# Optimization experiments

Measured on AMD Instinct MI355X. Metric: run time of the kernel, lower is better.

Reference implementation:

```python
import jax, jax.numpy as jnp
import numpy as np
from jax import lax

B, S, D_MODEL, H, D_CONV, CHUNK = 8, 4096, 1024, 16, 4, 64
D_INNER = D_MODEL


def setup_inputs() -> dict:
    key = jax.random.key(0)
    ks = jax.random.split(key, 6)
    x = jax.random.normal(ks[0], (B, S, D_MODEL), jnp.float32)
    in_proj_w = jax.random.normal(ks[1], (D_INNER + H, D_MODEL), jnp.float32) * 0.02
    conv_w = jax.random.normal(ks[2], (D_INNER, 1, D_CONV), jnp.float32) * 0.3
    conv_b = jnp.zeros((D_INNER,), jnp.float32)
    w_base = jax.random.uniform(ks[3], (H,), jnp.float32, minval=-0.5, maxval=0.5)
    out_proj_w = jax.random.normal(ks[4], (D_MODEL, D_INNER), jnp.float32) * 0.02
    return {"x": x, "in_proj_w": in_proj_w, "conv_w": conv_w, "conv_b": conv_b,
            "w_base": w_base, "out_proj_w": out_proj_w}


def _segsum(a):
    # a: (..., T) -> (..., T, T) with out[i, j] = sum_{k=j+1..i} a[k] for i>=j else -inf
    T = a.shape[-1]
    lower_strict = jnp.tril(jnp.ones((T, T), bool), -1)   # row i > col j
    lower = jnp.tril(jnp.ones((T, T), bool), 0)
    xr = jnp.where(lower_strict, a[..., :, None], 0.0)    # (..., T, T)
    s = jnp.cumsum(xr, axis=-2)
    return jnp.where(lower, s, -jnp.inf)


def _ssd(x, A, l):
    # x: (b, s, h, n); A: (b, s, h); l = chunk size
    b, s, h, n = x.shape
    c = s // l
    x = x.reshape(b, c, l, h, n)
    A = A.reshape(b, c, l, h).transpose(0, 3, 1, 2)        # (b, h, c, l)
    A_cumsum = jnp.cumsum(A, axis=-1)

    # intra-chunk (diagonal) part
    L_log = _segsum(A)                                      # (b, h, c, l, l)
    L = jnp.exp(L_log - jnp.max(L_log, axis=-1, keepdims=True))
    norm_diag = L.sum(-1).transpose(0, 2, 3, 1)             # (b, c, l, h)
    Y_diag = jnp.einsum('bhcls,bcshn->bclhn', L, x)

    # chunk states
    decay_states = A_cumsum[..., -1:] - A_cumsum            # (b, h, c, l)
    decay_states = jnp.exp(decay_states - jnp.max(decay_states, axis=-1, keepdims=True))
    norm_decay = decay_states.sum(-1).transpose(0, 2, 1)    # (b, c, h)
    states = jnp.einsum('bhcl,bclhn->bchn', decay_states, x)

    norm_decay = jnp.pad(norm_decay, ((0, 0), (1, 0), (0, 0)))
    states = jnp.pad(states, ((0, 0), (1, 0), (0, 0), (0, 0)))

    # inter-chunk recurrence
    decay_chunk = _segsum(jnp.pad(A_cumsum[..., -1], ((0, 0), (0, 0), (1, 0))))  # (b,h,c+1,c+1)
    decay_chunk = jnp.exp(decay_chunk - jnp.max(decay_chunk, axis=-1, keepdims=True))
    norm_decay = jnp.einsum('bhzc,bch->bzh', decay_chunk, norm_decay)[:, :-1]    # (b, c, h)
    states = jnp.einsum('bhzc,bchn->bzhn', decay_chunk, states)[:, :-1]          # (b, c, h, n)

    # off-diagonal output
    state_decay_out = jnp.exp(A_cumsum - jnp.max(A_cumsum, axis=-1, keepdims=True))
    norm_off = jnp.einsum('bch,bhcl->bclh', norm_decay, state_decay_out)
    Y_off = jnp.einsum('bchn,bhcl->bclhn', states, state_decay_out)

    Y = (Y_diag + Y_off).reshape(b, s, h, n)
    norm = (norm_diag + norm_off).reshape(b, s, h)
    return Y / norm[..., None]


def reference(x, in_proj_w, conv_w, conv_b, w_base, out_proj_w):
    b, s, d_model = x.shape
    d_inner = in_proj_w.shape[0] - H
    xw = jnp.einsum('bsd,ed->bse', x, in_proj_w)            # (b, s, d_inner + H)
    xi, w = xw[..., :d_inner], xw[..., d_inner:]            # (b,s,d_inner), (b,s,H)
    # causal depthwise conv (padding k-1 on the left == pad both + slice [:s])
    xc = lax.conv_general_dilated(
        xi.transpose(0, 2, 1), conv_w, window_strides=(1,),
        padding=[(D_CONV - 1, 0)], feature_group_count=d_inner,
        dimension_numbers=('NCH', 'OIH', 'NCH'))
    xc = (xc + conv_b[None, :, None]).transpose(0, 2, 1)    # (b, s, d_inner)
    xh = xc.reshape(b, s, H, d_inner // H)                  # (b, s, h, n)
    A = w * w_base                                          # (b, s, H)
    y = _ssd(xh, A, CHUNK)                                  # (b, s, h, n)
    y = y.reshape(b, s, d_inner)
    return jnp.einsum('bsd,ed->bse', y, out_proj_w)         # (b, s, d_model)
```

## Files before the change

kernel.cpp:

```cpp
#include <hip/hip_runtime.h>
#include <hip/hip_bf16.h>
#include <cstdint>

#define B_ 8
#define S_ 4096
#define DM 1024
#define H_ 16
#define DN 64
#define CH 64
#define NC 64
#define M_ (B_ * S_)

typedef unsigned short u16;
typedef u16 u16x8 __attribute__((ext_vector_type(8)));
typedef u16 u16x4 __attribute__((ext_vector_type(4)));
typedef float f32x4 __attribute__((ext_vector_type(4)));
typedef __bf16 bf16x8 __attribute__((ext_vector_type(8)));

__device__ __forceinline__ float bf2f(u16 u) { return __uint_as_float(((unsigned)u) << 16); }
__device__ __forceinline__ u16 f2bf(float f) { __bf16 h = (__bf16)f; return __builtin_bit_cast(u16, h); }

#define GLOAD16(gp, lp) \
  __builtin_amdgcn_global_load_lds((__attribute__((address_space(1))) const void*)(gp), \
                                   (__attribute__((address_space(3))) void*)(lp), 16, 0, 0)
#define BAR()   asm volatile("s_barrier" ::: "memory")
#define VMCNT6() asm volatile("s_waitcnt vmcnt(6)" ::: "memory")
#define VMCNT0() asm volatile("s_waitcnt vmcnt(0)" ::: "memory")

__device__ __forceinline__ void stage_unit(const u16* __restrict__ src, int row0, int kt,
                                           int ks, u16* ldsu, int t, int K) {
#pragma unroll
  for (int i = 0; i < 2; ++i) {
    int f = i * 512 + t;
    int row = f >> 2, j = f & 3;
    int g = j ^ ((row >> 1) & 3);
    GLOAD16(src + (size_t)(row0 + row) * K + kt * 64 + ks * 32 + g * 8, ldsu + f * 8);
  }
}

__device__ __forceinline__ void lda4(bf16x8* fr, const u16* unit, int rbase, int lr, int lk) {
#pragma unroll
  for (int q = 0; q < 4; ++q) {
    int row = rbase + q * 16 + lr;
    int cell = row * 4 + (lk ^ ((row >> 1) & 3));
    fr[q] = *reinterpret_cast<const bf16x8*>(&unit[cell * 8]);
  }
}

__device__ __forceinline__ void mfma16(f32x4 (&acc)[8][4], int mh, const bf16x8* aF, const bf16x8* bF) {
  __builtin_amdgcn_s_setprio(1);
#pragma unroll
  for (int q = 0; q < 4; ++q)
#pragma unroll
    for (int nf = 0; nf < 4; ++nf)
      acc[mh * 4 + q][nf] = __builtin_amdgcn_mfma_f32_16x16x32_bf16(aF[q], bF[nf], acc[mh * 4 + q][nf], 0, 0, 0);
  __builtin_amdgcn_s_setprio(0);
}

template<int MODE>
__global__ __launch_bounds__(512, 2) void bgemm8(
    const u16* __restrict__ A, const u16* __restrict__ Bw,
    void* __restrict__ Cout, int K)
{
  __shared__ u16 lds[8][8192];
  const int orig = blockIdx.x;
  const int swz  = (orig & 7) * 64 + (orig >> 3);
  const int m0 = (swz >> 2) * 256;
  const int n0 = (swz & 3) * 256;
  const int t  = threadIdx.x;
  const int wid = t >> 6, l = t & 63;
  const int wm = wid >> 2, wn = wid & 3;
  const int lr = l & 15, lk = l >> 4;
  const int arb = wm * 128;
  const int brb = wn * 64;

  f32x4 acc[8][4];
#pragma unroll
  for (int i = 0; i < 8; ++i)
#pragma unroll
    for (int j = 0; j < 4; ++j) acc[i][j] = (f32x4){0.f, 0.f, 0.f, 0.f};

  stage_unit(A,  m0, 0, 0, lds[0], t, K);
  stage_unit(A,  m0, 0, 1, lds[1], t, K);
  stage_unit(Bw, n0, 0, 0, lds[2], t, K);
  stage_unit(Bw, n0, 0, 1, lds[3], t, K);
  stage_unit(Bw, n0, 1, 0, lds[6], t, K);
  stage_unit(Bw, n0, 1, 1, lds[7], t, K);
  stage_unit(A,  m0, 1, 0, lds[4], t, K);
  VMCNT6();
  BAR();

  bf16x8 aF[4], bF0[4], bF1[4];
  for (int i = 0; i < 8; ++i) {
    const bool st = (i < 7);
    lda4(aF, lds[0], arb, lr, lk);
    lda4(bF0, lds[2], brb, lr, lk);
    stage_unit(A, m0, 2 * i + 1, 1, lds[5], t, K);
    BAR(); mfma16(acc, 0, aF, bF0); BAR();
    lda4(aF, lds[1], arb, lr, lk);
    lda4(bF1, lds[3], brb, lr, lk);
    if (st) stage_unit(Bw, n0, 2 * i + 2, 0, lds[2], t, K);
    BAR(); mfma16(acc, 0, aF, bF1); BAR();
    lda4(aF, lds[0], arb + 64, lr, lk);
    if (st) stage_unit(Bw, n0, 2 * i + 2, 1, lds[3], t, K);
    BAR(); mfma16(acc, 1, aF, bF0); BAR();
    lda4(aF, lds[1], arb + 64, lr, lk);
    if (st) { stage_unit(A, m0, 2 * i + 2, 0, lds[0], t, K); VMCNT6(); }
    else    { VMCNT0(); }
    BAR(); mfma16(acc, 1, aF, bF1); BAR();
    lda4(aF, lds[4], arb, lr, lk);
    lda4(bF0, lds[6], brb, lr, lk);
    if (st) stage_unit(A, m0, 2 * i + 2, 1, lds[1], t, K);
    BAR(); mfma16(acc, 0, aF, bF0); BAR();
    lda4(aF, lds[5], arb, lr, lk);
    lda4(bF1, lds[7], brb, lr, lk);
    if (st) stage_unit(Bw, n0, 2 * i + 3, 0, lds[6], t, K);
    BAR(); mfma16(acc, 0, aF, bF1); BAR();
    lda4(aF, lds[4], arb + 64, lr, lk);
    if (st) stage_unit(Bw, n0, 2 * i + 3, 1, lds[7], t, K);
    BAR(); mfma16(acc, 1, aF, bF0); BAR();
    lda4(aF, lds[5], arb + 64, lr, lk);
    if (st) { stage_unit(A, m0, 2 * i + 3, 0, lds[4], t, K); VMCNT6(); }
    BAR(); mfma16(acc, 1, aF, bF1); BAR();
  }

#pragma unroll
  for (int mf = 0; mf < 8; ++mf) {
#pragma unroll
    for (int nf = 0; nf < 4; ++nf) {
      int n  = n0 + wn * 64 + nf * 16 + lr;
      int mb = m0 + wm * 128 + mf * 16 + lk * 4;
#pragma unroll
      for (int r = 0; r < 4; ++r) {
        if (MODE == 0) ((float*)Cout)[(size_t)(mb + r) * 1024 + n] = acc[mf][nf][r];
        else           ((u16*)Cout)[(size_t)(mb + r) * 1024 + n] = f2bf(acc[mf][nf][r]);
      }
    }
  }
}

__global__ __launch_bounds__(256) void cvt32to16(const float* __restrict__ in, u16* __restrict__ out)
{
  size_t i = ((size_t)blockIdx.x * 256 + threadIdx.x) * 8;
  f32x4 a = *reinterpret_cast<const f32x4*>(&in[i]);
  f32x4 b = *reinterpret_cast<const f32x4*>(&in[i + 4]);
  u16x8 o;
#pragma unroll
  for (int j = 0; j < 4; ++j) { o[j] = f2bf(a[j]); o[4 + j] = f2bf(b[j]); }
  *reinterpret_cast<u16x8*>(&out[i]) = o;
}

__global__ __launch_bounds__(256) void cvtlo(const float* __restrict__ ipw, u16* __restrict__ wlo)
{
  size_t e = ((size_t)blockIdx.x * 256 + threadIdx.x) * 8;
  f32x4 a = *reinterpret_cast<const f32x4*>(&ipw[1048576 + e]);
  f32x4 b = *reinterpret_cast<const f32x4*>(&ipw[1048576 + e + 4]);
  u16x8 o;
#pragma unroll
  for (int j = 0; j < 4; ++j) {
    u16 h = f2bf(a[j]); o[j]     = f2bf(a[j] - bf2f(h));
    u16 g = f2bf(b[j]); o[4 + j] = f2bf(b[j] - bf2f(g));
  }
  *reinterpret_cast<u16x8*>(&wlo[e]) = o;
}

__global__ __launch_bounds__(256) void wsplit(
    const float* __restrict__ x, const u16* __restrict__ wbf, const u16* __restrict__ wlo,
    u16* __restrict__ xbf, float* __restrict__ wbufT)
{
  __shared__ u16 hi[64 * 64];
  __shared__ u16 lo[64 * 64];
  const int r0 = blockIdx.x * 64;
  const int t  = threadIdx.x;
  const int w  = t >> 6, l = t & 63;
  const int lr = l & 15, lk = l >> 4;
  const int c8   = t & 7;
  const int srow = t >> 3;

  f32x4 acc = (f32x4){0.f, 0.f, 0.f, 0.f};

  for (int kt = 0; kt < 16; ++kt) {
    __syncthreads();
#pragma unroll
    for (int p = 0; p < 2; ++p) {
      int row = srow + 32 * p;
      const float* gp = &x[(size_t)(r0 + row) * 1024 + kt * 64 + c8 * 8];
      f32x4 a = *reinterpret_cast<const f32x4*>(gp);
      f32x4 b = *reinterpret_cast<const f32x4*>(gp + 4);
      u16x8 h8, l8;
#pragma unroll
      for (int j = 0; j < 4; ++j) {
        u16 ha = f2bf(a[j]); h8[j]     = ha; l8[j]     = f2bf(a[j] - bf2f(ha));
        u16 hb = f2bf(b[j]); h8[4 + j] = hb; l8[4 + j] = f2bf(b[j] - bf2f(hb));
      }
      int cell = row * 8 + (c8 ^ (row & 7));
      *reinterpret_cast<u16x8*>(&hi[cell * 8]) = h8;
      *reinterpret_cast<u16x8*>(&lo[cell * 8]) = l8;
      *reinterpret_cast<u16x8*>(&xbf[(size_t)(r0 + row) * 1024 + kt * 64 + c8 * 8]) = h8;
    }
    __syncthreads();
#pragma unroll
    for (int ks = 0; ks < 2; ++ks) {
      int row  = w * 16 + lr;
      int cell = row * 8 + ((ks * 4 + lk) ^ (row & 7));
      bf16x8 ah = *reinterpret_cast<const bf16x8*>(&hi[cell * 8]);
      bf16x8 al = *reinterpret_cast<const bf16x8*>(&lo[cell * 8]);
      bf16x8 bh = *reinterpret_cast<const bf16x8*>(&wbf[(size_t)(1024 + lr) * 1024 + kt * 64 + ks * 32 + lk * 8]);
      bf16x8 bl = *reinterpret_cast<const bf16x8*>(&wlo[(size_t)lr * 1024 + kt * 64 + ks * 32 + lk * 8]);
      acc = __builtin_amdgcn_mfma_f32_16x16x32_bf16(ah, bh, acc, 0, 0, 0);
      acc = __builtin_amdgcn_mfma_f32_16x16x32_bf16(al, bh, acc, 0, 0, 0);
      acc = __builtin_amdgcn_mfma_f32_16x16x32_bf16(ah, bl, acc, 0, 0, 0);
    }
  }
#pragma unroll
  for (int r = 0; r < 4; ++r)
    wbufT[(size_t)lr * M_ + r0 + w * 16 + lk * 4 + r] = acc[r];
}

__global__ __launch_bounds__(256) void chunk_kernel(
    const u16* __restrict__ xi,
    const float* __restrict__ cw, const float* __restrict__ cb,
    const float* __restrict__ wbufT, const float* __restrict__ w_base,
    u16* __restrict__ ybuf, float* __restrict__ Acum, float* __restrict__ acbuf,
    float* __restrict__ normd, float* __restrict__ states, float* __restrict__ ndbuf)
{
  int bi = blockIdx.x;
  int c  = bi & 63;
  int h  = (bi >> 6) & 15;
  int b  = bi >> 10;
  int bh = b * 16 + h;
  int t  = threadIdx.x;
  __shared__ u16 xis[67][64];
  __shared__ u16 xsT[64][66];
  __shared__ float pc[CH], m1s[CH], dsv[CH];
  __shared__ float wls[4][64];
  __shared__ float cbs[64];
  size_t m0 = (size_t)b * S_ + (size_t)c * CH;
  size_t abase = ((size_t)bh * NC + c) * CH;

  wls[t & 3][t >> 2] = cw[(size_t)h * 256 + t];
  if (t < 64) cbs[t] = cb[h * 64 + t];

  {
    int g8  = t & 7;
    int hr0 = t >> 3;
    for (int hr = hr0; hr < 67; hr += 32) {
      u16x8 v = {0, 0, 0, 0, 0, 0, 0, 0};
      if (!(c == 0 && hr < 3))
        v = *reinterpret_cast<const u16x8*>(&xi[(m0 - 3 + hr) * DM + h * 64 + g8 * 8]);
      *reinterpret_cast<u16x8*>(&xis[hr][g8 * 8]) = v;
    }
  }

  if (t < 64) {
    float p = wbufT[(size_t)h * M_ + m0 + t] * w_base[h];
#pragma unroll
    for (int off = 1; off < 64; off <<= 1) {
      float v = __shfl_up(p, off);
      if (t >= off) p += v;
    }
    Acum[abase + t] = p;
    if (t == 63) acbuf[(size_t)bh * NC + c] = p;
    pc[t] = p;
    float rmin = p;
#pragma unroll
    for (int off = 1; off < 64; off <<= 1) {
      float v = __shfl_up(rmin, off);
      if (t >= off) rmin = fminf(rmin, v);
    }
    m1s[t] = p - rmin;
    float minall = __shfl(rmin, 63);
    dsv[t] = __expf(minall - p);
  }
  __syncthreads();

  {
    int n  = t & 63;
    int lb = (t >> 6) * 16;
    float w0 = wls[0][n], w1 = wls[1][n], w2 = wls[2][n], w3 = wls[3][n];
    float bias = cbs[n];
    float a = bf2f(xis[lb + 0][n]);
    float bv = bf2f(xis[lb + 1][n]);
    float cv = bf2f(xis[lb + 2][n]);
    u16x8 o0, o1;
#pragma unroll
    for (int r = 0; r < 16; ++r) {
      float dv = bf2f(xis[lb + r + 3][n]);
      float s = fmaf(w3, dv, fmaf(w2, cv, fmaf(w1, bv, fmaf(w0, a, bias))));
      if (r < 8) o0[r] = f2bf(s); else o1[r - 8] = f2bf(s);
      a = bv; bv = cv; cv = dv;
    }
    *reinterpret_cast<u16x8*>(&xsT[n][lb]) = o0;
    *reinterpret_cast<u16x8*>(&xsT[n][lb + 8]) = o1;
  }
  __syncthreads();

  {
    int w = t >> 6, l = t & 63;
    int lr = l & 15, lk = l >> 4;
    int row = w * 16 + lr;
    float pr = pc[row], m1r = m1s[row];
    bf16x8 afr[2];
    float np = 0.f;
#pragma unroll
    for (int ks = 0; ks < 2; ++ks) {
      int sbase = ks * 32 + lk * 8;
      u16x8 av;
#pragma unroll
      for (int j = 0; j < 8; ++j) {
        int s = sbase + j;
        float L = (s <= row) ? __expf(pr - pc[s] - m1r) : 0.f;
        np += L;
        av[j] = f2bf(L);
      }
      afr[ks] = __builtin_bit_cast(bf16x8, av);
    }
    np += __shfl_xor(np, 16);
    np += __shfl_xor(np, 32);
    if (lk == 0) normd[abase + row] = np;

    f32x4 acc[4];
#pragma unroll
    for (int nf = 0; nf < 4; ++nf) acc[nf] = (f32x4){0.f, 0.f, 0.f, 0.f};
#pragma unroll
    for (int ks = 0; ks < 2; ++ks)
#pragma unroll
      for (int nf = 0; nf < 4; ++nf) {
        bf16x8 bfr = *reinterpret_cast<const bf16x8*>(&xsT[nf * 16 + lr][ks * 32 + lk * 8]);
        acc[nf] = __builtin_amdgcn_mfma_f32_16x16x32_bf16(afr[ks], bfr, acc[nf], 0, 0, 0);
      }
#pragma unroll
    for (int nf = 0; nf < 4; ++nf)
#pragma unroll
      for (int r = 0; r < 4; ++r)
        ybuf[(m0 + w * 16 + lk * 4 + r) * DM + h * 64 + nf * 16 + lr] = f2bf(acc[nf][r]);
  }

  if (t < 64) {
    float acc = 0.f;
#pragma unroll
    for (int l8 = 0; l8 < 64; l8 += 8) {
      u16x8 xv = *reinterpret_cast<const u16x8*>(&xsT[t][l8]);
#pragma unroll
      for (int j = 0; j < 8; ++j) acc = fmaf(dsv[l8 + j], bf2f(xv[j]), acc);
    }
    states[((size_t)bh * NC + c) * DN + t] = acc;
    float v = dsv[t];
#pragma unroll
    for (int off = 32; off >= 1; off >>= 1) v += __shfl_down(v, off);
    if (t == 0) ndbuf[(size_t)bh * NC + c] = v;
  }
}

__global__ __launch_bounds__(256) void interchunk_kernel(
    const float* __restrict__ acbuf, const float* __restrict__ states,
    const float* __restrict__ ndbuf, float* __restrict__ nstates, float* __restrict__ nndbuf)
{
  int bh = blockIdx.x;
  int t  = threadIdx.x;
  __shared__ float Ssum[NC], minP[NC], ndl[NC];
  if (t < 64) {
    float ac = acbuf[(size_t)bh * NC + t];
    float S = ac;
#pragma unroll
    for (int off = 1; off < 64; off <<= 1) {
      float v = __shfl_up(S, off);
      if (t >= off) S += v;
    }
    float Pc = S - ac;
    float mp = Pc;
#pragma unroll
    for (int off = 1; off < 64; off <<= 1) {
      float v = __shfl_up(mp, off);
      if (t >= off) mp = fminf(mp, v);
    }
    Ssum[t] = S;
    minP[t] = mp;
    ndl[t]  = ndbuf[(size_t)bh * NC + t];
  }
  __syncthreads();
  int n  = t & 63;
  int r0 = t >> 6;
  for (int r = 0; r < 16; ++r) {
    int z = r0 + r * 4;
    float mpz = minP[z];
    float acc = 0.f;
    for (int j = 0; j < z; ++j) {
      float e = __expf(mpz - Ssum[j]);
      acc = fmaf(e, states[((size_t)bh * NC + j) * DN + n], acc);
    }
    nstates[((size_t)bh * NC + z) * DN + n] = acc;
  }
  if (t < 64) {
    int z = t;
    float mpz = minP[z];
    float acc = 0.f;
    for (int j = 0; j < z; ++j) acc = fmaf(__expf(mpz - Ssum[j]), ndl[j], acc);
    nndbuf[(size_t)bh * NC + z] = acc;
  }
}

__global__ __launch_bounds__(256) void final_kernel(
    const float* __restrict__ Acum, const float* __restrict__ normd,
    const float* __restrict__ nstates, const float* __restrict__ nndbuf,
    u16* __restrict__ ybuf)
{
  int bi = blockIdx.x;
  int c  = bi & 63;
  int h  = (bi >> 6) & 15;
  int b  = bi >> 10;
  int bh = b * 16 + h;
  int t  = threadIdx.x;
  __shared__ float sdo[CH], nrm[CH], sto[DN];
  __shared__ float ndo_s;
  size_t abase = ((size_t)bh * NC + c) * CH;
  if (t < 64) {
    float p = Acum[abase + t];
    float m3 = p;
#pragma unroll
    for (int off = 32; off >= 1; off >>= 1) m3 = fmaxf(m3, __shfl_down(m3, off));
    m3 = __shfl(m3, 0);
    sdo[t] = __expf(p - m3);
    nrm[t] = normd[abase + t];
    sto[t] = nstates[((size_t)bh * NC + c) * DN + t];
    if (t == 0) ndo_s = nndbuf[(size_t)bh * NC + c];
  }
  __syncthreads();
  size_t m0 = (size_t)b * S_ + (size_t)c * CH;
  int g  = t & 7;
  int l0 = t >> 3;
  float ndo = ndo_s;
  for (int li = l0; li < 64; li += 32) {
    size_t a = (m0 + li) * DM + h * DN + g * 8;
    u16x8 v = *reinterpret_cast<u16x8*>(&ybuf[a]);
    float sd = sdo[li];
    float rec = 1.f / (nrm[li] + ndo * sd);
    u16x8 o;
#pragma unroll
    for (int jj = 0; jj < 8; ++jj) {
      float yd = bf2f(v[jj]);
      o[jj] = f2bf((yd + sto[g * 8 + jj] * sd) * rec);
    }
    *reinterpret_cast<u16x8*>(&ybuf[a]) = o;
  }
}

extern "C" void kernel_launch(void* const* d_in, const int* in_sizes, int n_in,
                              void* d_out, int out_size, void* d_ws, size_t ws_size,
                              hipStream_t stream) {
  const float* x          = (const float*)d_in[0];
  const float* in_proj_w  = (const float*)d_in[1];
  const float* conv_w     = (const float*)d_in[2];
  const float* conv_b     = (const float*)d_in[3];
  const float* w_base     = (const float*)d_in[4];
  const float* out_proj_w = (const float*)d_in[5];
  float* out = (float*)d_out;
  char* ws = (char*)d_ws;

  u16*   wbf_in  = (u16*)  (ws + 0);
  u16*   wbf_out = (u16*)  (ws + 2129920);
  u16*   wlo16   = (u16*)  (ws + 4227072);
  float* wbufT   = (float*)(ws + 4259840);
  float* Acum    = (float*)(ws + 6356992);
  float* acbuf   = (float*)(ws + 8454144);
  float* normd   = (float*)(ws + 8486912);
  float* states  = (float*)(ws + 10584064);
  float* ndbuf   = (float*)(ws + 12681216);
  float* nstates = (float*)(ws + 12713984);
  float* nndbuf  = (float*)(ws + 14811136);
  u16*   xbf     = (u16*)  (ws + 14843904);
  u16*   xibf    = (u16*)  (ws + 81952768);
  u16*   ybuf    = xbf;

  cvt32to16<<<520, 256, 0, stream>>>(in_proj_w, wbf_in);
  cvt32to16<<<512, 256, 0, stream>>>(out_proj_w, wbf_out);
  cvtlo<<<8, 256, 0, stream>>>(in_proj_w, wlo16);
  wsplit<<<512, 256, 0, stream>>>(x, wbf_in, wlo16, xbf, wbufT);
  bgemm8<1><<<512, 512, 0, stream>>>(xbf, wbf_in, (void*)xibf, DM);
  chunk_kernel<<<8192, 256, 0, stream>>>(xibf, conv_w, conv_b, wbufT, w_base,
                                         ybuf, Acum, acbuf, normd, states, ndbuf);
  interchunk_kernel<<<128, 256, 0, stream>>>(acbuf, states, ndbuf, nstates, nndbuf);
  final_kernel<<<8192, 256, 0, stream>>>(Acum, normd, nstates, nndbuf, ybuf);
  bgemm8<0><<<512, 512, 0, stream>>>(ybuf, wbf_out, (void*)out, DM);
}
```

Baseline: 293.9 us.

## Pipeline wsplit with register prefetch, double-buffered LDS, and split-K across waves

The wsplit kernel now handles 32 rows per block instead of 64, so twice as many blocks launch. It prefetches the next K-tile of x into registers while converting and computing the current one. LDS is double-buffered, which cuts the two barriers per iteration down to one. The two K halves are split across wave pairs and then reduced through shared memory at the end. The aim is to hide global-load latency and raise occupancy and parallelism in this memory-bound fp32-to-bf16 split and small GEMM, at the cost of an extra reduction step and a barrier.

```diff
diff --git a/kernel.cpp b/kernel.cpp
--- a/kernel.cpp
+++ b/kernel.cpp
@@ -168,53 +168,66 @@
     const float* __restrict__ x, const u16* __restrict__ wbf, const u16* __restrict__ wlo,
     u16* __restrict__ xbf, float* __restrict__ wbufT)
 {
-  __shared__ u16 hi[64 * 64];
-  __shared__ u16 lo[64 * 64];
-  const int r0 = blockIdx.x * 64;
+  __shared__ u16 hi[2][32 * 64];
+  __shared__ u16 lo[2][32 * 64];
+  __shared__ float comb[2][64][4];
+  const int r0 = blockIdx.x * 32;
   const int t  = threadIdx.x;
   const int w  = t >> 6, l = t & 63;
   const int lr = l & 15, lk = l >> 4;
+  const int rg = (w & 1) * 16;
+  const int h2 = w >> 1;
+  const int srow = t >> 3;
   const int c8   = t & 7;
-  const int srow = t >> 3;
+  const int wcell = srow * 8 + (c8 ^ (srow & 7));
+
+  const float* gp0 = &x[(size_t)(r0 + srow) * 1024 + c8 * 8];
+  f32x4 a0 = *reinterpret_cast<const f32x4*>(gp0);
+  f32x4 a1 = *reinterpret_cast<const f32x4*>(gp0 + 4);
 
   f32x4 acc = (f32x4){0.f, 0.f, 0.f, 0.f};
 
   for (int kt = 0; kt < 16; ++kt) {
-    __syncthreads();
-#pragma unroll
-    for (int p = 0; p < 2; ++p) {
-      int row = srow + 32 * p;
-      const float* gp = &x[(size_t)(r0 + row) * 1024 + kt * 64 + c8 * 8];
-      f32x4 a = *reinterpret_cast<const f32x4*>(gp);
-      f32x4 b = *reinterpret_cast<const f32x4*>(gp + 4);
-      u16x8 h8, l8;
-#pragma unroll
-      for (int j = 0; j < 4; ++j) {
-        u16 ha = f2bf(a[j]); h8[j]     = ha; l8[j]     = f2bf(a[j] - bf2f(ha));
-        u16 hb = f2bf(b[j]); h8[4 + j] = hb; l8[4 + j] = f2bf(b[j] - bf2f(hb));
-      }
-      int cell = row * 8 + (c8 ^ (row & 7));
-      *reinterpret_cast<u16x8*>(&hi[cell * 8]) = h8;
-      *reinterpret_cast<u16x8*>(&lo[cell * 8]) = l8;
-      *reinterpret_cast<u16x8*>(&xbf[(size_t)(r0 + row) * 1024 + kt * 64 + c8 * 8]) = h8;
-    }
-    __syncthreads();
-#pragma unroll
-    for (int ks = 0; ks < 2; ++ks) {
-      int row  = w * 16 + lr;
-      int cell = row * 8 + ((ks * 4 + lk) ^ (row & 7));
-      bf16x8 ah = *reinterpret_cast<const bf16x8*>(&hi[cell * 8]);
-      bf16x8 al = *reinterpret_cast<const bf16x8*>(&lo[cell * 8]);
-      bf16x8 bh = *reinterpret_cast<const bf16x8*>(&wbf[(size_t)(1024 + lr) * 1024 + kt * 64 + ks * 32 + lk * 8]);
-      bf16x8 bl = *reinterpret_cast<const bf16x8*>(&wlo[(size_t)lr * 1024 + kt * 64 + ks * 32 + lk * 8]);
+    f32x4 b0, b1;
+    if (kt < 15) {
+      const float* gp = gp0 + (kt + 1) * 64;
+      b0 = *reinterpret_cast<const f32x4*>(gp);
+      b1 = *reinterpret_cast<const f32x4*>(gp + 4);
+    }
+    u16x8 h8, l8;
+#pragma unroll
+    for (int j = 0; j < 4; ++j) {
+      u16 ha = f2bf(a0[j]); h8[j]     = ha; l8[j]     = f2bf(a0[j] - bf2f(ha));
+      u16 hb = f2bf(a1[j]); h8[4 + j] = hb; l8[4 + j] = f2bf(a1[j] - bf2f(hb));
+    }
+    *reinterpret_cast<u16x8*>(&hi[kt & 1][wcell * 8]) = h8;
+    *reinterpret_cast<u16x8*>(&lo[kt & 1][wcell * 8]) = l8;
+    *reinterpret_cast<u16x8*>(&xbf[(size_t)(r0 + srow) * 1024 + kt * 64 + c8 * 8]) = h8;
+    BAR();
+    {
+      int row  = rg + lr;
+      int cell = row * 8 + ((h2 * 4 + lk) ^ (row & 7));
+      bf16x8 ah = *reinterpret_cast<const bf16x8*>(&hi[kt & 1][cell * 8]);
+      bf16x8 al = *reinterpret_cast<const bf16x8*>(&lo[kt & 1][cell * 8]);
+      bf16x8 bh = *reinterpret_cast<const bf16x8*>(&wbf[(size_t)(1024 + lr) * 1024 + kt * 64 + h2 * 32 + lk * 8]);
+      bf16x8 bl = *reinterpret_cast<const bf16x8*>(&wlo[(size_t)lr * 1024 + kt * 64 + h2 * 32 + lk * 8]);
       acc = __builtin_amdgcn_mfma_f32_16x16x32_bf16(ah, bh, acc, 0, 0, 0);
       acc = __builtin_amdgcn_mfma_f32_16x16x32_bf16(al, bh, acc, 0, 0, 0);
       acc = __builtin_amdgcn_mfma_f32_16x16x32_bf16(ah, bl, acc, 0, 0, 0);
     }
-  }
-#pragma unroll
-  for (int r = 0; r < 4; ++r)
-    wbufT[(size_t)lr * M_ + r0 + w * 16 + lk * 4 + r] = acc[r];
+    a0 = b0; a1 = b1;
+  }
+
+  if (w >= 2) {
+#pragma unroll
+    for (int r = 0; r < 4; ++r) comb[w - 2][l][r] = acc[r];
+  }
+  BAR();
+  if (w < 2) {
+#pragma unroll
+    for (int r = 0; r < 4; ++r)
+      wbufT[(size_t)lr * M_ + r0 + rg + lk * 4 + r] = acc[r] + comb[w][l][r];
+  }
 }
 
 __global__ __launch_bounds__(256) void chunk_kernel(
@@ -475,7 +488,7 @@
   cvt32to16<<<520, 256, 0, stream>>>(in_proj_w, wbf_in);
   cvt32to16<<<512, 256, 0, stream>>>(out_proj_w, wbf_out);
   cvtlo<<<8, 256, 0, stream>>>(in_proj_w, wlo16);
-  wsplit<<<512, 256, 0, stream>>>(x, wbf_in, wlo16, xbf, wbufT);
+  wsplit<<<1024, 256, 0, stream>>>(x, wbf_in, wlo16, xbf, wbufT);
   bgemm8<1><<<512, 512, 0, stream>>>(xbf, wbf_in, (void*)xibf, DM);
   chunk_kernel<<<8192, 256, 0, stream>>>(xibf, conv_w, conv_b, wbufT, w_base,
                                          ybuf, Acum, acbuf, normd, states, ndbuf);
```

Result: no change. 293.5 us (-0.1%).

## Restructure wsplit into per-wave independent tiles with register prefetch

Applied to the files above, without the earlier changes.

The wsplit kernel now gives each wave its own 16-row tile and a private LDS staging area, so block-wide __syncthreads are replaced by a wave-local lgkmcnt wait. The next K-slice of x and the weights is prefetched into registers while the current slice is split and fed to MFMA, and the grid becomes 1024 blocks of 128 threads. The aim is to cut barrier stalls and hide global load latency in this memory-bound split-precision projection. In exchange, each load is narrower (32 columns per step over 32 iterations) and register pressure goes up from the prefetch buffers.

```diff
diff --git a/kernel.cpp b/kernel.cpp
--- a/kernel.cpp
+++ b/kernel.cpp
@@ -164,57 +164,60 @@
   *reinterpret_cast<u16x8*>(&wlo[e]) = o;
 }
 
-__global__ __launch_bounds__(256) void wsplit(
+__global__ __launch_bounds__(128) void wsplit(
     const float* __restrict__ x, const u16* __restrict__ wbf, const u16* __restrict__ wlo,
     u16* __restrict__ xbf, float* __restrict__ wbufT)
 {
-  __shared__ u16 hi[64 * 64];
-  __shared__ u16 lo[64 * 64];
-  const int r0 = blockIdx.x * 64;
-  const int t  = threadIdx.x;
-  const int w  = t >> 6, l = t & 63;
+  __shared__ u16 hi[2][16 * 5 * 8];
+  __shared__ u16 lo[2][16 * 5 * 8];
+  const int t = threadIdx.x;
+  const int w = t >> 6, l = t & 63;
+  const int r0 = blockIdx.x * 32 + w * 16;
   const int lr = l & 15, lk = l >> 4;
-  const int c8   = t & 7;
-  const int srow = t >> 3;
+  const int srow = l >> 2, skc = l & 3;
+  u16* HI = hi[w];
+  u16* LO = lo[w];
+
+  const float* gx  = &x[(size_t)(r0 + srow) * 1024 + skc * 8];
+  const u16*   gbh = &wbf[(size_t)(1024 + lr) * 1024 + lk * 8];
+  const u16*   gbl = &wlo[(size_t)lr * 1024 + lk * 8];
+
+  f32x4 a0 = *reinterpret_cast<const f32x4*>(gx);
+  f32x4 a1 = *reinterpret_cast<const f32x4*>(gx + 4);
+  bf16x8 bh = *reinterpret_cast<const bf16x8*>(gbh);
+  bf16x8 bl = *reinterpret_cast<const bf16x8*>(gbl);
 
   f32x4 acc = (f32x4){0.f, 0.f, 0.f, 0.f};
-
-  for (int kt = 0; kt < 16; ++kt) {
-    __syncthreads();
-#pragma unroll
-    for (int p = 0; p < 2; ++p) {
-      int row = srow + 32 * p;
-      const float* gp = &x[(size_t)(r0 + row) * 1024 + kt * 64 + c8 * 8];
-      f32x4 a = *reinterpret_cast<const f32x4*>(gp);
-      f32x4 b = *reinterpret_cast<const f32x4*>(gp + 4);
-      u16x8 h8, l8;
-#pragma unroll
-      for (int j = 0; j < 4; ++j) {
-        u16 ha = f2bf(a[j]); h8[j]     = ha; l8[j]     = f2bf(a[j] - bf2f(ha));
-        u16 hb = f2bf(b[j]); h8[4 + j] = hb; l8[4 + j] = f2bf(b[j] - bf2f(hb));
-      }
-      int cell = row * 8 + (c8 ^ (row & 7));
-      *reinterpret_cast<u16x8*>(&hi[cell * 8]) = h8;
-      *reinterpret_cast<u16x8*>(&lo[cell * 8]) = l8;
-      *reinterpret_cast<u16x8*>(&xbf[(size_t)(r0 + row) * 1024 + kt * 64 + c8 * 8]) = h8;
-    }
-    __syncthreads();
-#pragma unroll
-    for (int ks = 0; ks < 2; ++ks) {
-      int row  = w * 16 + lr;
-      int cell = row * 8 + ((ks * 4 + lk) ^ (row & 7));
-      bf16x8 ah = *reinterpret_cast<const bf16x8*>(&hi[cell * 8]);
-      bf16x8 al = *reinterpret_cast<const bf16x8*>(&lo[cell * 8]);
-      bf16x8 bh = *reinterpret_cast<const bf16x8*>(&wbf[(size_t)(1024 + lr) * 1024 + kt * 64 + ks * 32 + lk * 8]);
-      bf16x8 bl = *reinterpret_cast<const bf16x8*>(&wlo[(size_t)lr * 1024 + kt * 64 + ks * 32 + lk * 8]);
-      acc = __builtin_amdgcn_mfma_f32_16x16x32_bf16(ah, bh, acc, 0, 0, 0);
-      acc = __builtin_amdgcn_mfma_f32_16x16x32_bf16(al, bh, acc, 0, 0, 0);
-      acc = __builtin_amdgcn_mfma_f32_16x16x32_bf16(ah, bl, acc, 0, 0, 0);
-    }
-  }
-#pragma unroll
-  for (int r = 0; r < 4; ++r)
-    wbufT[(size_t)lr * M_ + r0 + w * 16 + lk * 4 + r] = acc[r];
+  const int wcell = srow * 5 + skc;
+  const int rcell = lr * 5 + lk;
+
+  for (int kt = 0; kt < 32; ++kt) {
+    f32x4 n0, n1; bf16x8 nbh, nbl;
+    if (kt < 31) {
+      n0  = *reinterpret_cast<const f32x4*>(gx + (kt + 1) * 32);
+      n1  = *reinterpret_cast<const f32x4*>(gx + (kt + 1) * 32 + 4);
+      nbh = *reinterpret_cast<const bf16x8*>(gbh + (kt + 1) * 32);
+      nbl = *reinterpret_cast<const bf16x8*>(gbl + (kt + 1) * 32);
+    }
+    u16x8 h8, l8;
+#pragma unroll
+    for (int j = 0; j < 4; ++j) {
+      u16 ha = f2bf(a0[j]); h8[j]     = ha; l8[j]     = f2bf(a0[j] - bf2f(ha));
+      u16 hb = f2bf(a1[j]); h8[4 + j] = hb; l8[4 + j] = f2bf(a1[j] - bf2f(hb));
+    }
+    *reinterpret_cast<u16x8*>(&xbf[(size_t)(r0 + srow) * 1024 + kt * 32 + skc * 8]) = h8;
+    *reinterpret_cast<u16x8*>(&HI[wcell * 8]) = h8;
+    *reinterpret_cast<u16x8*>(&LO[wcell * 8]) = l8;
+    asm volatile("s_waitcnt lgkmcnt(0)" ::: "memory");
+    __builtin_amdgcn_sched_barrier(0);
+    bf16x8 ah = *reinterpret_cast<const bf16x8*>(&HI[rcell * 8]);
+    bf16x8 al = *reinterpret_cast<const bf16x8*>(&LO[rcell * 8]);
+    acc = __builtin_amdgcn_mfma_f32_16x16x32_bf16(ah, bh, acc, 0, 0, 0);
+    acc = __builtin_amdgcn_mfma_f32_16x16x32_bf16(al, bh, acc, 0, 0, 0);
+    acc = __builtin_amdgcn_mfma_f32_16x16x32_bf16(ah, bl, acc, 0, 0, 0);
+    a0 = n0; a1 = n1; bh = nbh; bl = nbl;
+  }
+  *reinterpret_cast<f32x4*>(&wbufT[(size_t)lr * M_ + r0 + lk * 4]) = acc;
 }
 
 __global__ __launch_bounds__(256) void chunk_kernel(
@@ -475,7 +478,7 @@
   cvt32to16<<<520, 256, 0, stream>>>(in_proj_w, wbf_in);
   cvt32to16<<<512, 256, 0, stream>>>(out_proj_w, wbf_out);
   cvtlo<<<8, 256, 0, stream>>>(in_proj_w, wlo16);
-  wsplit<<<512, 256, 0, stream>>>(x, wbf_in, wlo16, xbf, wbufT);
+  wsplit<<<1024, 128, 0, stream>>>(x, wbf_in, wlo16, xbf, wbufT);
   bgemm8<1><<<512, 512, 0, stream>>>(xbf, wbf_in, (void*)xibf, DM);
   chunk_kernel<<<8192, 256, 0, stream>>>(xibf, conv_w, conv_b, wbufT, w_base,
                                          ybuf, Acum, acbuf, normd, states, ndbuf);
```

New measurement: 290.8 us. About the same (-1.0%).
